# Kernel optimization log

Measured on AMD Instinct MI355X. Metric: run time of the kernel, lower is better.

## Reference

```python
import jax, jax.numpy as jnp
import numpy as np

N, DZ, L, H, MLPH, INC = 256, 256, 256, 512, 2048, 8
CAT_IDX = np.arange(0, 192, 2)                      # 96 categorical token positions (interleaved)
NUM_IDX = np.setdiff1d(np.arange(L), CAT_IDX)       # 160 numerical token positions
CARDS = [4, 16, 128]                                # cardinality per categorical group
GSZ = 32                                            # tokens per categorical group
NUM_CARD = 100                                      # cardinality of quantized numerical params


def setup_inputs() -> dict:
    ks = list(jax.random.split(jax.random.key(0), 24))
    def nrm(shape, s=0.02):
        return jax.random.normal(ks.pop(), shape, jnp.float32) * s
    inp = {}
    inp['z'] = jax.random.normal(ks.pop(), (N, DZ), jnp.float32)
    inp['mlp_w0'] = nrm((DZ, MLPH)); inp['mlp_b0'] = jnp.zeros((MLPH,), jnp.float32)
    inp['mlp_w1'] = nrm((MLPH, MLPH)); inp['mlp_b1'] = jnp.zeros((MLPH,), jnp.float32)
    inp['mlp_w2'] = nrm((MLPH, MLPH)); inp['mlp_b2'] = jnp.zeros((MLPH,), jnp.float32)
    inp['conv_w'] = nrm((H, INC)); inp['conv_b'] = jnp.zeros((H,), jnp.float32)
    for g, card in enumerate(CARDS):
        inp[f'cat_w{g}'] = nrm((H, card)); inp[f'cat_b{g}'] = jnp.zeros((card,), jnp.float32)
    inp['num_w'] = nrm((H, 2)); inp['num_b'] = jnp.zeros((2,), jnp.float32)
    inp['num_target'] = jax.random.uniform(ks.pop(), (N, len(NUM_IDX)), jnp.float32)
    inp['cat_target'] = jax.random.randint(ks.pop(), (N, len(CAT_IDX)), 0, 4, jnp.int32)
    return inp


def reference(z, mlp_w0, mlp_b0, mlp_w1, mlp_b1, mlp_w2, mlp_b2, conv_w, conv_b,
              cat_w0, cat_b0, cat_w1, cat_b1, cat_w2, cat_b2, num_w, num_b,
              num_target, cat_target):
    n = z.shape[0]
    # MLP: fc0 -> act -> fc1 -> act -> fc2
    h = z @ mlp_w0 + mlp_b0
    h = jax.nn.relu(h) @ mlp_w1 + mlp_b1
    h = jax.nn.relu(h) @ mlp_w2 + mlp_b2
    h = h.reshape(n, INC, L)                        # (N, C=8, L)
    # act + 1x1 conv to hidden_size, then transpose -> (N, L, H)
    u = jnp.einsum('ncl,hc->nlh', jax.nn.relu(h), conv_w) + conv_b
    # ---- categorical tokens: gather, per-cardinality heads, CE NLL, argmax sample ----
    hc = u[:, CAT_IDX, :]                           # (N, 96, H)
    heads = [(cat_w0, cat_b0), (cat_w1, cat_b1), (cat_w2, cat_b2)]
    nlls, samps = [], []
    for g, (w, b) in enumerate(heads):
        hg = hc[:, g * GSZ:(g + 1) * GSZ, :]        # (N, 32, H)
        logits = hg @ w + b                         # (N, 32, card)
        logp = jax.nn.log_softmax(logits, axis=-1)
        tg = cat_target[:, g * GSZ:(g + 1) * GSZ]
        nlls.append(-jnp.take_along_axis(logp, tg[..., None], axis=-1)[..., 0])
        samps.append(jnp.argmax(logits, axis=-1))
    cat_nll = jnp.concatenate(nlls, axis=1)         # (N, 96)
    cat_samples = jnp.concatenate(samps, axis=1)    # (N, 96)
    # ---- numerical tokens: gather, 2-param discretized logistic, NLL, mode sample ----
    hn = u[:, NUM_IDX, :]                           # (N, 160, H)
    p = hn @ num_w + num_b                          # (N, 160, 2)
    mu = jax.nn.sigmoid(p[..., 0])
    s = jax.nn.softplus(p[..., 1]) + 1e-4
    hb = 1.0 / (2.0 * (NUM_CARD - 1))               # half bin width
    t = num_target
    cdf_p = jax.nn.sigmoid((t + hb - mu) / s)
    cdf_m = jax.nn.sigmoid((t - hb - mu) / s)
    prob = jnp.where(t < hb, cdf_p, jnp.where(t > 1.0 - hb, 1.0 - cdf_m, cdf_p - cdf_m))
    num_nll = -jnp.log(jnp.maximum(prob, 1e-7))     # (N, 160)
    num_samples = jax.lax.stop_gradient(jnp.round(mu * (NUM_CARD - 1)) / (NUM_CARD - 1))
    # ---- scatter samples back into the preallocated output tensor ----
    u_out = jnp.zeros((n, L, 3), jnp.float32)
    u_out = u_out.at[:, CAT_IDX, 0].set(cat_samples.astype(jnp.float32))
    u_out = u_out.at[:, NUM_IDX, 1].set(num_samples)
    return u_out, cat_nll, num_nll
```

## Files before the change

kernel.cpp:

```cpp
#include <hip/hip_runtime.h>
#include <hip/hip_fp16.h>
#include <math.h>

#define NN   256
#define LL   256
#define HH   512
#define MLPHv 2048
#define INCv 8
#define NCOLS 150

typedef _Float16 f16x8 __attribute__((ext_vector_type(8)));
typedef float    f32x4 __attribute__((ext_vector_type(4)));
typedef unsigned short ushort_t;

__device__ __forceinline__ void split1(float f, ushort_t& h, ushort_t& l)
{
    __half hh = __float2half_rn(f);
    h = __half_as_ushort(hh);
    l = __half_as_ushort(__float2half_rn((f - __half2float(hh)) * 4096.f));
}

__device__ __forceinline__ void pack8(const float* fv, uint4& hv, uint4& lv)
{
    ushort_t h[8], l[8];
#pragma unroll
    for (int j = 0; j < 8; ++j) split1(fv[j], h[j], l[j]);
    hv.x = (unsigned)h[0] | ((unsigned)h[1] << 16);
    hv.y = (unsigned)h[2] | ((unsigned)h[3] << 16);
    hv.z = (unsigned)h[4] | ((unsigned)h[5] << 16);
    hv.w = (unsigned)h[6] | ((unsigned)h[7] << 16);
    lv.x = (unsigned)l[0] | ((unsigned)l[1] << 16);
    lv.y = (unsigned)l[2] | ((unsigned)l[3] << 16);
    lv.z = (unsigned)l[4] | ((unsigned)l[5] << 16);
    lv.w = (unsigned)l[6] | ((unsigned)l[7] << 16);
}

typedef __attribute__((address_space(3))) unsigned int lds_u32;
typedef __attribute__((address_space(1))) const unsigned int glb_u32;
__device__ __forceinline__ void gl_lds16(const ushort_t* g, ushort_t* l)
{
    __builtin_amdgcn_global_load_lds((glb_u32*)g, (lds_u32*)l, 16, 0, 0);
}
__device__ __forceinline__ void gl_lds16f(const float* g, float* l)
{
    __builtin_amdgcn_global_load_lds((glb_u32*)g, (lds_u32*)l, 16, 0, 0);
}


__global__ __launch_bounds__(256) void prep_small(
    const float* __restrict__ z,
    const float* __restrict__ cvw, const float* __restrict__ cvb,
    const float* __restrict__ cw0, const float* __restrict__ cb0,
    const float* __restrict__ cw1, const float* __restrict__ cb1,
    const float* __restrict__ cw2, const float* __restrict__ cb2,
    const float* __restrict__ nw,  const float* __restrict__ nbv,
    ushort_t* __restrict__ zh, ushort_t* __restrict__ zl,
    float* __restrict__ Mf, float* __restrict__ beta)
{
    const int bid = blockIdx.x;
    const int tid = threadIdx.x;
    if (bid < 16) {
        const int idx = bid * 256 + tid;
        const int r = idx >> 4, kq = idx & 15;
        const float* p = z + (size_t)r * 256 + kq * 16;
        float fv[16];
#pragma unroll
        for (int q = 0; q < 4; ++q) {
            float4 v = *(const float4*)(p + q * 4);
            fv[q * 4 + 0] = v.x; fv[q * 4 + 1] = v.y;
            fv[q * 4 + 2] = v.z; fv[q * 4 + 3] = v.w;
        }
        const int gm = r >> 4, l16 = r & 15;
#pragma unroll
        for (int o = 0; o < 2; ++o) {
            uint4 hv, lv;
            pack8(&fv[o * 8], hv, lv);
            const int koct = kq * 2 + o;
            const int ks = koct >> 2, koct3 = koct & 3;
            const size_t off = ((size_t)(gm * 8 + ks) * 64 + l16 + (koct3 << 4)) * 8;
            *(uint4*)&zh[off] = hv;
            *(uint4*)&zl[off] = lv;
        }
    } else {
        const int k = bid - 16;
        const float* W; const float* B; int off, card;
        if (k < 4)        { W = cw0; B = cb0; off = 0;   card = 4;   }
        else if (k < 20)  { W = cw1; B = cb1; off = 4;   card = 16;  }
        else if (k < 148) { W = cw2; B = cb2; off = 20;  card = 128; }
        else              { W = nw;  B = nbv; off = 148; card = 2;   }
        const int kc = k - off;
        float part[INCv + 1];
#pragma unroll
        for (int c = 0; c <= INCv; ++c) part[c] = 0.f;
#pragma unroll
        for (int it = 0; it < 2; ++it) {
            const int h = tid + it * 256;
            const float wv = W[h * card + kc];
#pragma unroll
            for (int c = 0; c < INCv; ++c) part[c] += cvw[h * INCv + c] * wv;
            part[INCv] += cvb[h] * wv;
        }
        __shared__ float red[INCv + 1][4];
        const int lane = tid & 63, wave = tid >> 6;
#pragma unroll
        for (int c = 0; c <= INCv; ++c) {
            float v = part[c];
#pragma unroll
            for (int o = 32; o >= 1; o >>= 1) v += __shfl_down(v, o, 64);
            if (lane == 0) red[c][wave] = v;
        }
        __syncthreads();
        if (tid <= INCv) {
            const float s = red[tid][0] + red[tid][1] + red[tid][2] + red[tid][3];
            if (tid < INCv) Mf[tid * NCOLS + k] = s;
            else            beta[k] = s + B[kc];
        }
    }
}

template <int OUT>
__global__ __launch_bounds__(512, 1) void gemm_wf(
    const ushort_t* __restrict__ Ah, const ushort_t* __restrict__ Al,
    const float* __restrict__ W, const float* __restrict__ bias,
    float* __restrict__ part, ushort_t* __restrict__ oH, ushort_t* __restrict__ oL,
    int KS32, int kchunk32, int steps)
{
    __shared__ ushort_t sAh[2][8192];
    __shared__ ushort_t sAl[2][8192];
    __shared__ float    sWf[2][4160];
    __shared__ ushort_t sWh[2][4096];
    __shared__ ushort_t sWl[2][4096];

    const int tid  = threadIdx.x;
    const int lane = tid & 63, w = tid >> 6;
    const int wr   = w >> 1, wc = w & 1;
    const int bx   = blockIdx.x, by = blockIdx.y, bz = blockIdx.z;
    const int bn   = bx * 64;
    const int kb0  = bz * kchunk32;

    f32x4 accH[2][2], accC[2][2];
#pragma unroll
    for (int r = 0; r < 2; ++r)
#pragma unroll
        for (int c = 0; c < 2; ++c) {
            accH[r][c] = (f32x4){0.f, 0.f, 0.f, 0.f};
            accC[r][c] = (f32x4){0.f, 0.f, 0.f, 0.f};
        }

    auto STAGE = [&](int ts, int b) {
        const int kb = kb0 + ts * 2;
#pragma unroll
        for (int i = 0; i < 2; ++i) {
            const int run = w + i * 8;
            const int g = run >> 1, ks = run & 1;
            const size_t f = ((size_t)(by * 8 + g) * KS32 + kb + ks) * 512 + lane * 8;
            gl_lds16(Ah + f, &sAh[b][run * 512]);
            gl_lds16(Al + f, &sAl[b][run * 512]);
        }
        const int k0 = kb * 32;
#pragma unroll
        for (int ii = 0; ii < 2; ++ii) {
            const int i = w * 2 + ii;
            const float* src = W + (size_t)(k0 + i * 4 + (lane >> 4)) * 2048 + bn + (lane & 15) * 4;
            gl_lds16f(src, &sWf[b][i * 260]);
        }
    };

    STAGE(0, 0);
    for (int t = 0; t < steps; ++t) {
        const int cur = t & 1;
        if (t + 1 < steps) {
            STAGE(t + 1, cur ^ 1);
            asm volatile("s_waitcnt vmcnt(6)" ::: "memory");
        } else {
            asm volatile("s_waitcnt vmcnt(0)" ::: "memory");
        }
        __builtin_amdgcn_s_barrier();
        asm volatile("" ::: "memory");

        {
            const int col = lane;
            const int i0  = w * 2;
            float fv[8];
#pragma unroll
            for (int j = 0; j < 4; ++j) fv[j]     = sWf[cur][i0 * 260 + j * 64 + col];
#pragma unroll
            for (int j = 0; j < 4; ++j) fv[4 + j] = sWf[cur][(i0 + 1) * 260 + j * 64 + col];
            uint4 hv, lv;
            pack8(fv, hv, lv);
            const int g = col >> 4, l16 = col & 15;
            const int ks = w >> 2, koct = w & 3;
            const int ub = ((g * 2 + ks) * 64 + l16 + koct * 16) * 8;
            *(uint4*)&sWh[cur][ub] = hv;
            *(uint4*)&sWl[cur][ub] = lv;
        }
        asm volatile("s_waitcnt lgkmcnt(0)" ::: "memory");
        __builtin_amdgcn_s_barrier();
        asm volatile("" ::: "memory");

#pragma unroll
        for (int ks = 0; ks < 2; ++ks) {
            f16x8 aH[2], aL[2], bHf[2], bLf[2];
#pragma unroll
            for (int r = 0; r < 2; ++r) {
                const int off = (((wr * 2 + r) * 2 + ks) * 64 + lane) * 8;
                aH[r] = *(const f16x8*)&sAh[cur][off];
                aL[r] = *(const f16x8*)&sAl[cur][off];
            }
#pragma unroll
            for (int c = 0; c < 2; ++c) {
                const int off = (((wc * 2 + c) * 2 + ks) * 64 + lane) * 8;
                bHf[c] = *(const f16x8*)&sWh[cur][off];
                bLf[c] = *(const f16x8*)&sWl[cur][off];
            }
#pragma unroll
            for (int r = 0; r < 2; ++r)
#pragma unroll
                for (int c = 0; c < 2; ++c) {
                    accH[r][c] = __builtin_amdgcn_mfma_f32_16x16x32_f16(aH[r], bHf[c], accH[r][c], 0, 0, 0);
                    accC[r][c] = __builtin_amdgcn_mfma_f32_16x16x32_f16(aH[r], bLf[c], accC[r][c], 0, 0, 0);
                    accC[r][c] = __builtin_amdgcn_mfma_f32_16x16x32_f16(aL[r], bHf[c], accC[r][c], 0, 0, 0);
                }
        }
        __builtin_amdgcn_s_barrier();
        asm volatile("" ::: "memory");
    }

    const float inv = 1.f / 4096.f;
#pragma unroll
    for (int r = 0; r < 2; ++r)
#pragma unroll
        for (int c = 0; c < 2; ++c) {
            const int row0 = by * 128 + (wr * 2 + r) * 16 + ((lane >> 4) << 2);
            const int col  = bn + (wc * 2 + c) * 16 + (lane & 15);
            if (OUT == 0) {
                float* po = part + (size_t)bz * 524288;
#pragma unroll
                for (int e = 0; e < 4; ++e)
                    po[(size_t)(row0 + e) * 2048 + col] = accH[r][c][e] + accC[r][c][e] * inv;
            } else {
                const float vb = bias[col];
                const int gm = (by * 8 + wr * 2 + r);
                const int ks = col >> 5, koct3 = (col >> 3) & 3, j = col & 7;
                const size_t fb = ((size_t)(gm * 64 + ks) * 64) * 8 + (koct3 << 4) * 8 + j;
#pragma unroll
                for (int e = 0; e < 4; ++e) {
                    const float v = fmaxf(accH[r][c][e] + accC[r][c][e] * inv + vb, 0.f);
                    ushort_t h, l;
                    split1(v, h, l);
                    const int l16 = ((lane >> 4) << 2) + e;
                    oH[fb + (size_t)l16 * 8] = h;
                    oL[fb + (size_t)l16 * 8] = l;
                }
            }
        }
}

__global__ __launch_bounds__(256) void reduce_pk(
    const float* __restrict__ part, const float* __restrict__ bias,
    ushort_t* __restrict__ oH, ushort_t* __restrict__ oL)
{
    const int b  = blockIdx.x;
    const int ct = b & 15, rg = b >> 4;
    const int e  = threadIdx.x * 4;
    const int row = rg * 8 + (e >> 7);
    const int col = ct * 128 + (e & 127);
    const size_t idx = (size_t)row * 2048 + col;
    float4 s = *(const float4*)&bias[col];
#pragma unroll
    for (int k = 0; k < 4; ++k) {
        const float4 p = *(const float4*)&part[(size_t)k * 524288 + idx];
        s.x += p.x; s.y += p.y; s.z += p.z; s.w += p.w;
    }
    s.x = fmaxf(s.x, 0.f); s.y = fmaxf(s.y, 0.f);
    s.z = fmaxf(s.z, 0.f); s.w = fmaxf(s.w, 0.f);
    ushort_t h[4], l[4];
    split1(s.x, h[0], l[0]); split1(s.y, h[1], l[1]);
    split1(s.z, h[2], l[2]); split1(s.w, h[3], l[3]);
    const int gm = row >> 4, l16 = row & 15;
    const int ks = col >> 5, koct3 = (col >> 3) & 3, j = col & 7;
    const size_t off = ((size_t)(gm * 64 + ks) * 64 + l16 + (koct3 << 4)) * 8 + j;
    ushort4 hv = {h[0], h[1], h[2], h[3]};
    ushort4 lv = {l[0], l[1], l[2], l[3]};
    *(ushort4*)&oH[off] = hv;
    *(ushort4*)&oL[off] = lv;
}

__global__ __launch_bounds__(256) void heads_kernel(
    const float* __restrict__ part, const float* __restrict__ b2,
    const float* __restrict__ Mf, const float* __restrict__ beta,
    const int* __restrict__ cat_target, const float* __restrict__ num_target,
    float* __restrict__ out)
{
    const int bx  = blockIdx.x;
    const int tid = threadIdx.x;
    __shared__ float Ms[INCv][128];
    __shared__ float Bsh[128];
    if (bx < 96) {
        const int g = bx >> 5;
        const int card = (g == 0) ? 4 : (g == 1) ? 16 : 128;
        const int off  = (g == 0) ? 0 : (g == 1) ? 4  : 20;
        for (int i = tid; i < card * INCv; i += 256) {
            int c = i / card, k = i % card;
            Ms[c][k] = Mf[c * NCOLS + off + k];
        }
        for (int i = tid; i < card; i += 256) Bsh[i] = beta[off + i];
        __syncthreads();

        const int idx = (bx & 31) * 256 + tid;
        const int n = idx >> 5, j = idx & 31;
        const int ci = g * 32 + j;
        const int l  = ci * 2;
        float rv[INCv];
#pragma unroll
        for (int c = 0; c < INCv; ++c) {
            const size_t e = (size_t)n * MLPHv + c * LL + l;
            float s = b2[c * LL + l];
#pragma unroll
            for (int k = 0; k < 4; ++k) s += part[(size_t)k * 524288 + e];
            rv[c] = fmaxf(s, 0.f);
        }

        float mx = -1e30f; int arg = 0;
        for (int k = 0; k < card; ++k) {
            float s = Bsh[k];
#pragma unroll
            for (int c = 0; c < INCv; ++c) s += rv[c] * Ms[c][k];
            if (s > mx) { mx = s; arg = k; }
        }
        const int tg = cat_target[n * 96 + ci];
        float sum = 0.f, stg = 0.f;
        for (int k = 0; k < card; ++k) {
            float s = Bsh[k];
#pragma unroll
            for (int c = 0; c < INCv; ++c) s += rv[c] * Ms[c][k];
            sum += expf(s - mx);
            if (k == tg) stg = s;
        }
        const float lse = mx + logf(sum);
        out[NN * LL * 3 + n * 96 + ci] = lse - stg;
        float* u = out + (size_t)(n * LL + l) * 3;
        u[0] = (float)arg; u[1] = 0.f; u[2] = 0.f;
    } else {
        const int idx = (bx - 96) * 256 + tid;
        const int n = idx / 160, ni = idx % 160;
        const int l = (ni < 96) ? (2 * ni + 1) : (96 + ni);
        float rv[INCv];
#pragma unroll
        for (int c = 0; c < INCv; ++c) {
            const size_t e = (size_t)n * MLPHv + c * LL + l;
            float s = b2[c * LL + l];
#pragma unroll
            for (int k = 0; k < 4; ++k) s += part[(size_t)k * 524288 + e];
            rv[c] = fmaxf(s, 0.f);
        }
        float p0 = beta[148], p1 = beta[149];
#pragma unroll
        for (int c = 0; c < INCv; ++c) {
            p0 += rv[c] * Mf[c * NCOLS + 148];
            p1 += rv[c] * Mf[c * NCOLS + 149];
        }
        const float mu = 1.f / (1.f + expf(-p0));
        const float sp = (p1 > 20.f) ? p1 : log1pf(expf(p1));
        const float s  = sp + 1e-4f;
        const float hb = 1.f / 198.f;
        const float t  = num_target[n * 160 + ni];
        const float cp = 1.f / (1.f + expf(-((t + hb - mu) / s)));
        const float cm = 1.f / (1.f + expf(-((t - hb - mu) / s)));
        const float prob = (t < hb) ? cp : ((t > 1.f - hb) ? (1.f - cm) : (cp - cm));
        out[NN * LL * 3 + NN * 96 + n * 160 + ni] = -logf(fmaxf(prob, 1e-7f));
        float* u = out + (size_t)(n * LL + l) * 3;
        u[0] = 0.f; u[1] = rintf(mu * 99.f) / 99.f; u[2] = 0.f;
    }
}

extern "C" void kernel_launch(void* const* d_in, const int* in_sizes, int n_in,
                              void* d_out, int out_size, void* d_ws, size_t ws_size,
                              hipStream_t stream)
{
    const float* z   = (const float*)d_in[0];
    const float* w0  = (const float*)d_in[1];
    const float* b0  = (const float*)d_in[2];
    const float* w1  = (const float*)d_in[3];
    const float* b1  = (const float*)d_in[4];
    const float* w2  = (const float*)d_in[5];
    const float* b2  = (const float*)d_in[6];
    const float* cvw = (const float*)d_in[7];
    const float* cvb = (const float*)d_in[8];
    const float* cw0 = (const float*)d_in[9];
    const float* cb0 = (const float*)d_in[10];
    const float* cw1 = (const float*)d_in[11];
    const float* cb1 = (const float*)d_in[12];
    const float* cw2 = (const float*)d_in[13];
    const float* cb2 = (const float*)d_in[14];
    const float* nw  = (const float*)d_in[15];
    const float* nb  = (const float*)d_in[16];
    const float* num_target = (const float*)d_in[17];
    const int*   cat_target = (const int*)d_in[18];
    float* out = (float*)d_out;
    float* ws  = (float*)d_ws;

    size_t o = 0;
    float*    part = ws + o;                o += 4ull * 524288;
    float*    Mf   = ws + o;                o += 1536;
    float*    beta = ws + o;                o += 256;
    ushort_t* zh   = (ushort_t*)(ws + o);   o += 32768;
    ushort_t* zl   = (ushort_t*)(ws + o);   o += 32768;
    ushort_t* r0h  = (ushort_t*)(ws + o);   o += 262144;
    ushort_t* r0l  = (ushort_t*)(ws + o);   o += 262144;
    ushort_t* r1h  = (ushort_t*)(ws + o);   o += 262144;
    ushort_t* r1l  = (ushort_t*)(ws + o);   o += 262144;

    prep_small<<<dim3(166), 256, 0, stream>>>(
        z, cvw, cvb, cw0, cb0, cw1, cb1, cw2, cb2, nw, nb, zh, zl, Mf, beta);

    gemm_wf<1><<<dim3(32, 2, 1), 512, 0, stream>>>(
        zh, zl, w0, b0, nullptr, r0h, r0l, 8, 8, 4);

    gemm_wf<0><<<dim3(32, 2, 4), 512, 0, stream>>>(
        r0h, r0l, w1, nullptr, part, nullptr, nullptr, 64, 16, 8);
    reduce_pk<<<dim3(512), 256, 0, stream>>>(part, b1, r1h, r1l);

    gemm_wf<0><<<dim3(32, 2, 4), 512, 0, stream>>>(
        r1h, r1l, w2, nullptr, part, nullptr, nullptr, 64, 16, 8);

    heads_kernel<<<dim3(256), 256, 0, stream>>>(
        part, b2, Mf, beta, cat_target, num_target, out);
}
```

Baseline: 73.73 us.

## Double GEMM block to 1024 threads, one 16-col tile per wave

The split-precision fp16 MFMA GEMM now launches 16 waves per block instead of 8, with each wave computing a 32x16 output tile rather than 32x32. Global-to-LDS staging and the fp32-to-fp16 weight split are spread across twice as many threads, and the packed weight buffer drops to a single LDS buffer. The goal is more latency hiding and less per-wave staging and conversion work. In exchange each block carries more barrier overhead, B fragments are no longer reused across two column tiles, and there are more waves per CU.

```diff
diff --git a/kernel.cpp b/kernel.cpp
--- a/kernel.cpp
+++ b/kernel.cpp
@@ -119,7 +119,7 @@
 }
 
 template <int OUT>
-__global__ __launch_bounds__(512, 1) void gemm_wf(
+__global__ __launch_bounds__(1024, 1) void gemm_w2(
     const ushort_t* __restrict__ Ah, const ushort_t* __restrict__ Al,
     const float* __restrict__ W, const float* __restrict__ bias,
     float* __restrict__ part, ushort_t* __restrict__ oH, ushort_t* __restrict__ oL,
@@ -128,42 +128,32 @@
     __shared__ ushort_t sAh[2][8192];
     __shared__ ushort_t sAl[2][8192];
     __shared__ float    sWf[2][4160];
-    __shared__ ushort_t sWh[2][4096];
-    __shared__ ushort_t sWl[2][4096];
+    __shared__ ushort_t sWh[4096];
+    __shared__ ushort_t sWl[4096];
 
     const int tid  = threadIdx.x;
     const int lane = tid & 63, w = tid >> 6;
-    const int wr   = w >> 1, wc = w & 1;
+    const int wr   = w >> 2, wc = w & 3;
     const int bx   = blockIdx.x, by = blockIdx.y, bz = blockIdx.z;
     const int bn   = bx * 64;
     const int kb0  = bz * kchunk32;
 
-    f32x4 accH[2][2], accC[2][2];
-#pragma unroll
-    for (int r = 0; r < 2; ++r)
-#pragma unroll
-        for (int c = 0; c < 2; ++c) {
-            accH[r][c] = (f32x4){0.f, 0.f, 0.f, 0.f};
-            accC[r][c] = (f32x4){0.f, 0.f, 0.f, 0.f};
-        }
+    f32x4 accH[2], accC[2];
+#pragma unroll
+    for (int r = 0; r < 2; ++r) {
+        accH[r] = (f32x4){0.f, 0.f, 0.f, 0.f};
+        accC[r] = (f32x4){0.f, 0.f, 0.f, 0.f};
+    }
 
     auto STAGE = [&](int ts, int b) {
         const int kb = kb0 + ts * 2;
-#pragma unroll
-        for (int i = 0; i < 2; ++i) {
-            const int run = w + i * 8;
-            const int g = run >> 1, ks = run & 1;
-            const size_t f = ((size_t)(by * 8 + g) * KS32 + kb + ks) * 512 + lane * 8;
-            gl_lds16(Ah + f, &sAh[b][run * 512]);
-            gl_lds16(Al + f, &sAl[b][run * 512]);
-        }
+        const int g = w >> 1, ks = w & 1;
+        const size_t fA = ((size_t)(by * 8 + g) * KS32 + kb + ks) * 512 + lane * 8;
+        gl_lds16(Ah + fA, &sAh[b][w * 512]);
+        gl_lds16(Al + fA, &sAl[b][w * 512]);
         const int k0 = kb * 32;
-#pragma unroll
-        for (int ii = 0; ii < 2; ++ii) {
-            const int i = w * 2 + ii;
-            const float* src = W + (size_t)(k0 + i * 4 + (lane >> 4)) * 2048 + bn + (lane & 15) * 4;
-            gl_lds16f(src, &sWf[b][i * 260]);
-        }
+        const float* src = W + (size_t)(k0 + w * 4 + (lane >> 4)) * 2048 + bn + (lane & 15) * 4;
+        gl_lds16f(src, &sWf[b][w * 260]);
     };
 
     STAGE(0, 0);
@@ -171,7 +161,7 @@
         const int cur = t & 1;
         if (t + 1 < steps) {
             STAGE(t + 1, cur ^ 1);
-            asm volatile("s_waitcnt vmcnt(6)" ::: "memory");
+            asm volatile("s_waitcnt vmcnt(3)" ::: "memory");
         } else {
             asm volatile("s_waitcnt vmcnt(0)" ::: "memory");
         }
@@ -179,20 +169,25 @@
         asm volatile("" ::: "memory");
 
         {
-            const int col = lane;
-            const int i0  = w * 2;
-            float fv[8];
-#pragma unroll
-            for (int j = 0; j < 4; ++j) fv[j]     = sWf[cur][i0 * 260 + j * 64 + col];
-#pragma unroll
-            for (int j = 0; j < 4; ++j) fv[4 + j] = sWf[cur][(i0 + 1) * 260 + j * 64 + col];
-            uint4 hv, lv;
-            pack8(fv, hv, lv);
-            const int g = col >> 4, l16 = col & 15;
-            const int ks = w >> 2, koct = w & 3;
-            const int ub = ((g * 2 + ks) * 64 + l16 + koct * 16) * 8;
-            *(uint4*)&sWh[cur][ub] = hv;
-            *(uint4*)&sWl[cur][ub] = lv;
+            const int col = tid & 63;
+            const int q   = tid >> 6;
+            const int ks  = q >> 3, koct3 = (q >> 1) & 3, hf = q & 1;
+            const int i   = ks * 8 + koct3 * 2 + hf;
+            float fv[4];
+#pragma unroll
+            for (int j = 0; j < 4; ++j) fv[j] = sWf[cur][i * 260 + j * 64 + col];
+            ushort_t h[4], l[4];
+#pragma unroll
+            for (int j = 0; j < 4; ++j) split1(fv[j], h[j], l[j]);
+            uint2 hv, lv;
+            hv.x = (unsigned)h[0] | ((unsigned)h[1] << 16);
+            hv.y = (unsigned)h[2] | ((unsigned)h[3] << 16);
+            lv.x = (unsigned)l[0] | ((unsigned)l[1] << 16);
+            lv.y = (unsigned)l[2] | ((unsigned)l[3] << 16);
+            const int g2 = col >> 4, l16 = col & 15;
+            const int ub = ((g2 * 2 + ks) * 64 + l16 + koct3 * 16) * 8 + hf * 4;
+            *(uint2*)&sWh[ub] = hv;
+            *(uint2*)&sWl[ub] = lv;
         }
         asm volatile("s_waitcnt lgkmcnt(0)" ::: "memory");
         __builtin_amdgcn_s_barrier();
@@ -200,27 +195,24 @@
 
 #pragma unroll
         for (int ks = 0; ks < 2; ++ks) {
-            f16x8 aH[2], aL[2], bHf[2], bLf[2];
+            f16x8 aH[2], aL[2], bHf, bLf;
 #pragma unroll
             for (int r = 0; r < 2; ++r) {
                 const int off = (((wr * 2 + r) * 2 + ks) * 64 + lane) * 8;
                 aH[r] = *(const f16x8*)&sAh[cur][off];
                 aL[r] = *(const f16x8*)&sAl[cur][off];
             }
-#pragma unroll
-            for (int c = 0; c < 2; ++c) {
-                const int off = (((wc * 2 + c) * 2 + ks) * 64 + lane) * 8;
-                bHf[c] = *(const f16x8*)&sWh[cur][off];
-                bLf[c] = *(const f16x8*)&sWl[cur][off];
+            {
+                const int off = ((wc * 2 + ks) * 64 + lane) * 8;
+                bHf = *(const f16x8*)&sWh[off];
+                bLf = *(const f16x8*)&sWl[off];
             }
 #pragma unroll
-            for (int r = 0; r < 2; ++r)
-#pragma unroll
-                for (int c = 0; c < 2; ++c) {
-                    accH[r][c] = __builtin_amdgcn_mfma_f32_16x16x32_f16(aH[r], bHf[c], accH[r][c], 0, 0, 0);
-                    accC[r][c] = __builtin_amdgcn_mfma_f32_16x16x32_f16(aH[r], bLf[c], accC[r][c], 0, 0, 0);
-                    accC[r][c] = __builtin_amdgcn_mfma_f32_16x16x32_f16(aL[r], bHf[c], accC[r][c], 0, 0, 0);
-                }
+            for (int r = 0; r < 2; ++r) {
+                accH[r] = __builtin_amdgcn_mfma_f32_16x16x32_f16(aH[r], bHf, accH[r], 0, 0, 0);
+                accC[r] = __builtin_amdgcn_mfma_f32_16x16x32_f16(aH[r], bLf, accC[r], 0, 0, 0);
+                accC[r] = __builtin_amdgcn_mfma_f32_16x16x32_f16(aL[r], bHf, accC[r], 0, 0, 0);
+            }
         }
         __builtin_amdgcn_s_barrier();
         asm volatile("" ::: "memory");
@@ -228,32 +220,30 @@
 
     const float inv = 1.f / 4096.f;
 #pragma unroll
-    for (int r = 0; r < 2; ++r)
-#pragma unroll
-        for (int c = 0; c < 2; ++c) {
-            const int row0 = by * 128 + (wr * 2 + r) * 16 + ((lane >> 4) << 2);
-            const int col  = bn + (wc * 2 + c) * 16 + (lane & 15);
-            if (OUT == 0) {
-                float* po = part + (size_t)bz * 524288;
-#pragma unroll
-                for (int e = 0; e < 4; ++e)
-                    po[(size_t)(row0 + e) * 2048 + col] = accH[r][c][e] + accC[r][c][e] * inv;
-            } else {
-                const float vb = bias[col];
-                const int gm = (by * 8 + wr * 2 + r);
-                const int ks = col >> 5, koct3 = (col >> 3) & 3, j = col & 7;
-                const size_t fb = ((size_t)(gm * 64 + ks) * 64) * 8 + (koct3 << 4) * 8 + j;
-#pragma unroll
-                for (int e = 0; e < 4; ++e) {
-                    const float v = fmaxf(accH[r][c][e] + accC[r][c][e] * inv + vb, 0.f);
-                    ushort_t h, l;
-                    split1(v, h, l);
-                    const int l16 = ((lane >> 4) << 2) + e;
-                    oH[fb + (size_t)l16 * 8] = h;
-                    oL[fb + (size_t)l16 * 8] = l;
-                }
+    for (int r = 0; r < 2; ++r) {
+        const int row0 = by * 128 + (wr * 2 + r) * 16 + ((lane >> 4) << 2);
+        const int col  = bn + wc * 16 + (lane & 15);
+        if (OUT == 0) {
+            float* po = part + (size_t)bz * 524288;
+#pragma unroll
+            for (int e = 0; e < 4; ++e)
+                po[(size_t)(row0 + e) * 2048 + col] = accH[r][e] + accC[r][e] * inv;
+        } else {
+            const float vb = bias[col];
+            const int gm = by * 8 + wr * 2 + r;
+            const int ks = col >> 5, koct3 = (col >> 3) & 3, j = col & 7;
+            const size_t fb = ((size_t)(gm * 64 + ks) * 64) * 8 + (koct3 << 4) * 8 + j;
+#pragma unroll
+            for (int e = 0; e < 4; ++e) {
+                const float v = fmaxf(accH[r][e] + accC[r][e] * inv + vb, 0.f);
+                ushort_t h, l;
+                split1(v, h, l);
+                const int l16 = ((lane >> 4) << 2) + e;
+                oH[fb + (size_t)l16 * 8] = h;
+                oL[fb + (size_t)l16 * 8] = l;
             }
         }
+    }
 }
 
 __global__ __launch_bounds__(256) void reduce_pk(
@@ -414,14 +404,14 @@
     prep_small<<<dim3(166), 256, 0, stream>>>(
         z, cvw, cvb, cw0, cb0, cw1, cb1, cw2, cb2, nw, nb, zh, zl, Mf, beta);
 
-    gemm_wf<1><<<dim3(32, 2, 1), 512, 0, stream>>>(
+    gemm_w2<1><<<dim3(32, 2, 1), 1024, 0, stream>>>(
         zh, zl, w0, b0, nullptr, r0h, r0l, 8, 8, 4);
 
-    gemm_wf<0><<<dim3(32, 2, 4), 512, 0, stream>>>(
+    gemm_w2<0><<<dim3(32, 2, 4), 1024, 0, stream>>>(
         r0h, r0l, w1, nullptr, part, nullptr, nullptr, 64, 16, 8);
     reduce_pk<<<dim3(512), 256, 0, stream>>>(part, b1, r1h, r1l);
 
-    gemm_wf<0><<<dim3(32, 2, 4), 512, 0, stream>>>(
+    gemm_w2<0><<<dim3(32, 2, 4), 1024, 0, stream>>>(
         r1h, r1l, w2, nullptr, part, nullptr, nullptr, 64, 16, 8);
 
     heads_kernel<<<dim3(256), 256, 0, stream>>>(
```

Result: no change. 72.85 us (-1.2%).
